# Optimization experiments

Hardware: AMD Instinct MI355X
Metric: run time of the kernel (lower is better)

## Reference

```python
import jax, jax.numpy as jnp
import numpy as np

B, H, W = 2, 64, 1024
C1, C2 = 64, 128
MLP = [128, 128]
KH, KW = 5, 5
NS = 3
DIST = 100.0
BN_EPS = 1e-5


def setup_inputs() -> dict:
    key = jax.random.key(0)
    ks = jax.random.split(key, 12)
    inp = {
        "xyz1_proj": jax.random.normal(ks[0], (B, H, W, 3), jnp.float32),
        "xyz2_proj": jax.random.normal(ks[1], (B, H, W, 3), jnp.float32),
        "feat1_proj": jax.random.normal(ks[2], (B, H, W, C1), jnp.float32),
        "feat2_proj": jax.random.normal(ks[3], (B, H, W, C2), jnp.float32),
    }
    cin = C1 + C2
    chans = [cin] + MLP
    for i in range(len(MLP)):
        inp[f"w{i}"] = jax.random.normal(ks[4 + 2 * i], (chans[i], chans[i + 1]), jnp.float32) * 0.05
        inp[f"b{i}"] = jnp.zeros((chans[i + 1],), jnp.float32)
        inp[f"g{i}"] = jnp.ones((chans[i + 1],), jnp.float32)
        inp[f"be{i}"] = jnp.zeros((chans[i + 1],), jnp.float32)
    return inp


def _grid_knn(xyz1, xyz2):
    """Structured-grid KNN (no_sort_knn): for each query pixel, scan a KHxKW
    window in row-major order and take the first NS in-bounds neighbors whose
    squared distance is below DIST^2. Returns flat neighbor indices (B,N,NS)
    and a validity mask (B,N,NS,1)."""
    b, h, w, _ = xyz1.shape
    n = h * w
    k = KH * KW
    x1 = xyz1.reshape(b, n, 3)
    x2 = xyz2.reshape(b, n, 3)
    oh = jnp.repeat(jnp.arange(KH) - KH // 2, KW)   # (K,)
    ow = jnp.tile(jnp.arange(KW) - KW // 2, KH)     # (K,)
    nh = jnp.arange(h)[:, None, None] + oh[None, None, :]   # (H,1,K)
    nw = jnp.arange(w)[None, :, None] + ow[None, None, :]   # (1,W,K)
    inb = ((nh >= 0) & (nh < h)) & ((nw >= 0) & (nw < w))    # (H,W,K)
    flat = jnp.clip(nh, 0, h - 1) * w + jnp.clip(nw, 0, w - 1)
    flat = jnp.broadcast_to(flat, (h, w, k)).reshape(n, k)
    inb = jnp.broadcast_to(inb, (h, w, k)).reshape(n, k)
    # window gather: (B,N,K,3)
    neigh = jnp.take(x2, flat.reshape(-1), axis=1).reshape(b, n, k, 3)
    sq = jnp.sum(jnp.square(neigh - x1[:, :, None, :]), -1)  # (B,N,K)
    valid = inb[None] & (sq < DIST * DIST)
    v = valid.astype(jnp.int32)
    rank = jnp.cumsum(v, -1) - v  # rank among valid, scan order
    sel, fnd = [], []
    for j in range(NS):
        hit = valid & (rank == j)
        sel.append(jnp.argmax(hit, -1))
        fnd.append(jnp.any(hit, -1))
    sel = jnp.stack(sel, -1)          # (B,N,NS) window slot
    found = jnp.stack(fnd, -1)        # (B,N,NS)
    flat_b = jnp.broadcast_to(flat[None], (b, n, k))
    sel_flat = jnp.take_along_axis(flat_b, sel, axis=-1)
    sel_flat = jnp.where(found, sel_flat, 0)  # zeros like the init buffers
    mask = found.astype(x1.dtype)[..., None]  # (B,N,NS,1)
    return sel_flat, mask


def _gather(feat_flat, sel_flat):
    # feat_flat: (B,N,C), sel_flat: (B,N,NS) -> (B,N,NS,C)
    b, n, c = feat_flat.shape
    idx = sel_flat.reshape(b, n * NS, 1)
    g = jnp.take_along_axis(feat_flat, jnp.broadcast_to(idx, (b, n * NS, c)), axis=1)
    return g.reshape(b, n, NS, c)


def reference(xyz1_proj, xyz2_proj, feat1_proj, feat2_proj,
              w0, b0, g0, be0, w1, b1, g1, be1):
    b, h, w, _ = xyz1_proj.shape
    n = h * w
    xyz1 = xyz1_proj.reshape(b, n, 3)
    xyz2 = xyz2_proj.reshape(b, n, 3)
    feat2 = feat2_proj.reshape(b, n, -1)

    sel_flat, mask = _grid_knn(xyz1_proj, xyz2_proj)
    mask = jax.lax.stop_gradient(mask)

    grouped_xyz = _gather(xyz2, sel_flat) * mask          # (B,N,NS,3)
    grouped_feat = _gather(feat2, sel_flat) * mask        # (B,N,NS,C2)

    dist = jnp.sum(jnp.square(grouped_xyz - xyz1[:, :, None, :]), -1)  # (B,N,NS)
    dist = jnp.where(dist < 1e-10, jnp.full_like(dist, 1e-10), dist)
    norm = jnp.sum(1.0 / dist, axis=2, keepdims=True)     # (B,N,1)
    weight = (1.0 / dist) / norm                          # (B,N,NS)
    interp = jnp.sum(grouped_feat * weight[..., None], axis=2)  # (B,N,C2)

    x = jnp.concatenate([feat1_proj.reshape(b, n, -1), interp], -1)  # (B,N,C1+C2)

    # 1x1 conv MLP with training-mode BatchNorm + ReLU
    for (wi, bi, gi, bei) in ((w0, b0, g0, be0), (w1, b1, g1, be1)):
        x = x @ wi + bi
        mu = jnp.mean(x, axis=(0, 1))
        var = jnp.var(x, axis=(0, 1))
        x = (x - mu) * jax.lax.rsqrt(var + BN_EPS) * gi + bei
        x = jax.nn.relu(x)
    return x  # (B, H*W, MLP[-1])
```

## Files before the change

### kernel.cpp

```cpp
#include <hip/hip_runtime.h>

#define H_    64
#define W_    1024
#define NPT   65536
#define NTOT  131072
#define C1_   64
#define C2_   128
#define CIN_  192
#define CM_   128
#define NS_   3
#define DIST2_ 10000.0f
#define BN_EPS_ 1e-5f
#define NSLOT 32

typedef __attribute__((ext_vector_type(8))) short short8;
typedef __attribute__((ext_vector_type(4))) float floatx4;

static __device__ __forceinline__ unsigned short f2bf(float f) {
    unsigned int u = __float_as_uint(f);
    u += 0x7fffu + ((u >> 16) & 1u);
    return (unsigned short)(u >> 16);
}
static __device__ __forceinline__ float bflo(unsigned u) { return __uint_as_float(u << 16); }
static __device__ __forceinline__ float bfhi(unsigned u) { return __uint_as_float(u & 0xffff0000u); }
static __device__ __forceinline__ unsigned packbf(float a, float b) {
    return (unsigned)f2bf(a) | ((unsigned)f2bf(b) << 16);
}

__global__ __launch_bounds__(256) void prep_knn_kernel(
    const float* __restrict__ w0, const float* __restrict__ w1,
    const float* __restrict__ xyz1, const float* __restrict__ xyz2,
    unsigned short* __restrict__ w0F, unsigned short* __restrict__ w1F,
    int* __restrict__ sel, float* __restrict__ wgt)
{
    const int blk = blockIdx.x;
    if (blk < 20) {
        int tid = blk * 256 + threadIdx.x;
        if (tid < 3072) {
            int c = tid, lane = c & 63, nt = (c >> 6) & 7, kk = c >> 9;
            int n = nt * 16 + (lane & 15);
            int kb = kk * 32 + (lane >> 4) * 8;
            #pragma unroll
            for (int j = 0; j < 8; j++)
                w0F[(size_t)c * 8 + j] = f2bf(w0[(size_t)(kb + j) * CM_ + n]);
        } else if (tid < 5120) {
            int c = tid - 3072, lane = c & 63, nt = (c >> 6) & 7, kk = c >> 9;
            int n = nt * 16 + (lane & 15);
            int kb = kk * 32 + (lane >> 4) * 8;
            #pragma unroll
            for (int j = 0; j < 8; j++)
                w1F[(size_t)c * 8 + j] = f2bf(w1[(size_t)(kb + j) * CM_ + n]);
        }
        return;
    }

    int pt = (blk - 20) * 256 + threadIdx.x;
    if (pt >= NTOT) return;
    int bidx = pt / NPT, n = pt % NPT;
    int h = n / W_, w = n % W_;

    const float* p1 = xyz1 + (size_t)pt * 3;
    float x1 = p1[0], y1 = p1[1], z1 = p1[2];
    const float* x2b = xyz2 + (size_t)bidx * NPT * 3;

    int   s0 = 0, s1 = 0, s2 = 0;
    float d0 = 0.f, d1 = 0.f, d2 = 0.f;
    int cnt = 0;
    for (int dh = -2; dh <= 2; dh++) {
        int nh = h + dh;
        bool okh = (nh >= 0) && (nh < H_);
        for (int dw = -2; dw <= 2; dw++) {
            int nw = w + dw;
            if (!(okh && nw >= 0 && nw < W_)) continue;
            int nidx = nh * W_ + nw;
            const float* p2 = x2b + (size_t)nidx * 3;
            float dx = p2[0] - x1, dy = p2[1] - y1, dz = p2[2] - z1;
            float sq = dx * dx + dy * dy + dz * dz;
            if (sq < DIST2_ && cnt < NS_) {
                if (cnt == 0)      { s0 = nidx; d0 = sq; }
                else if (cnt == 1) { s1 = nidx; d1 = sq; }
                else               { s2 = nidx; d2 = sq; }
                cnt++;
            }
        }
    }
    float self2 = x1 * x1 + y1 * y1 + z1 * z1;
    float dd0 = (cnt > 0) ? d0 : self2;
    float dd1 = (cnt > 1) ? d1 : self2;
    float dd2 = (cnt > 2) ? d2 : self2;
    dd0 = fmaxf(dd0, 1e-10f); dd1 = fmaxf(dd1, 1e-10f); dd2 = fmaxf(dd2, 1e-10f);
    float i0 = 1.0f / dd0, i1 = 1.0f / dd1, i2 = 1.0f / dd2;
    float norm = i0 + i1 + i2;
    sel[(size_t)pt * NS_ + 0] = (cnt > 0) ? s0 : 0;
    sel[(size_t)pt * NS_ + 1] = (cnt > 1) ? s1 : 0;
    sel[(size_t)pt * NS_ + 2] = (cnt > 2) ? s2 : 0;
    wgt[(size_t)pt * NS_ + 0] = (cnt > 0) ? i0 / norm : 0.f;
    wgt[(size_t)pt * NS_ + 1] = (cnt > 1) ? i1 / norm : 0.f;
    wgt[(size_t)pt * NS_ + 2] = (cnt > 2) ? i2 / norm : 0.f;
}

__global__ __launch_bounds__(256) void fused1_kernel(
    const float* __restrict__ feat1, const float* __restrict__ feat2,
    const int* __restrict__ sel, const float* __restrict__ wgt,
    const unsigned short* __restrict__ w0F, const float* __restrict__ b0,
    uint2* __restrict__ y0w, float* __restrict__ slots0)
{
    __shared__ unsigned short xstage[64][CIN_ + 8];
    __shared__ int   selL[64][NS_];
    __shared__ float wgtL[64][NS_];
    __shared__ float wsum[4][CM_], wsq[4][CM_];

    const int t = threadIdx.x;
    const int blk = blockIdx.x;
    const int pbase = blk * 64;
    const int bidx = blk >> 10;

    if (t < 64 * NS_) {
        ((int*)selL)[t]   = sel[(size_t)pbase * NS_ + t];
        ((float*)wgtL)[t] = wgt[(size_t)pbase * NS_ + t];
    }
    __syncthreads();

    #pragma unroll
    for (int i = 0; i < 4; i++) {
        int idx = t + i * 256;
        int p = idx >> 4, c4 = (idx & 15) << 2;
        float4 f = *(const float4*)(feat1 + (size_t)(pbase + p) * C1_ + c4);
        ushort4 u;
        u.x = f2bf(f.x); u.y = f2bf(f.y); u.z = f2bf(f.z); u.w = f2bf(f.w);
        *(ushort4*)&xstage[p][c4] = u;
    }
    const float* f2b = feat2 + (size_t)bidx * NPT * C2_;
    #pragma unroll
    for (int i = 0; i < 8; i++) {
        int idx = t + i * 256;
        int p = idx >> 5, c4 = (idx & 31) << 2;
        float ax = 0.f, ay = 0.f, az = 0.f, aw = 0.f;
        #pragma unroll
        for (int j = 0; j < NS_; j++) {
            float wj = wgtL[p][j];
            const float4 f = *(const float4*)(f2b + (size_t)selL[p][j] * C2_ + c4);
            ax += wj * f.x; ay += wj * f.y; az += wj * f.z; aw += wj * f.w;
        }
        ushort4 u;
        u.x = f2bf(ax); u.y = f2bf(ay); u.z = f2bf(az); u.w = f2bf(aw);
        *(ushort4*)&xstage[p][C1_ + c4] = u;
    }
    __syncthreads();

    const int wv = t >> 6, lane = t & 63;
    const int m = lane & 15, q = lane >> 4;
    const unsigned short* arow = &xstage[wv * 16 + m][q * 8];

    floatx4 acc[8];
    #pragma unroll
    for (int nt = 0; nt < 8; nt++) acc[nt] = (floatx4){0.f, 0.f, 0.f, 0.f};

    #pragma unroll
    for (int kk = 0; kk < 6; kk++) {
        short8 a = *(const short8*)(arow + kk * 32);
        #pragma unroll
        for (int nt = 0; nt < 8; nt++) {
            short8 bw = *(const short8*)(w0F + ((size_t)(kk * 8 + nt) * 64 + lane) * 8);
            acc[nt] = __builtin_amdgcn_mfma_f32_16x16x32_bf16(a, bw, acc[nt], 0, 0, 0);
        }
    }

    #pragma unroll
    for (int nt = 0; nt < 8; nt++) {
        int n = nt * 16 + m;
        float bv = b0[n];
        unsigned u0 = packbf(acc[nt][0] + bv, acc[nt][1] + bv);
        unsigned u1 = packbf(acc[nt][2] + bv, acc[nt][3] + bv);
        y0w[((size_t)(blk * 4 + wv) * 8 + nt) * 64 + lane] = make_uint2(u0, u1);
        float v0 = bflo(u0), v1 = bfhi(u0), v2 = bflo(u1), v3 = bfhi(u1);
        float s  = v0 + v1 + v2 + v3;
        float q2 = v0 * v0 + v1 * v1 + v2 * v2 + v3 * v3;
        s += __shfl_xor(s, 16, 64); q2 += __shfl_xor(q2, 16, 64);
        s += __shfl_xor(s, 32, 64); q2 += __shfl_xor(q2, 32, 64);
        if (q == 0) { wsum[wv][n] = s; wsq[wv][n] = q2; }
    }
    __syncthreads();

    float* slot = slots0 + (size_t)(blk & (NSLOT - 1)) * 256;
    if (t < CM_)
        atomicAdd(&slot[t], wsum[0][t] + wsum[1][t] + wsum[2][t] + wsum[3][t]);
    else
        atomicAdd(&slot[t], wsq[0][t - CM_] + wsq[1][t - CM_] + wsq[2][t - CM_] + wsq[3][t - CM_]);
}

__global__ __launch_bounds__(256) void fused2_kernel(
    const uint2* __restrict__ y0w, const float* __restrict__ slots0,
    const float* __restrict__ g0, const float* __restrict__ be0,
    const unsigned short* __restrict__ w1F, const float* __restrict__ b1,
    uint2* __restrict__ y1w, float* __restrict__ slots1)
{
    __shared__ unsigned short x1s[64][CM_ + 8];
    __shared__ float scl[CM_], shf[CM_];
    __shared__ float wsum[4][CM_], wsq[4][CM_];

    const int t = threadIdx.x;
    const int blk = blockIdx.x;

    if (t < CM_) {
        float s = 0.f, q2 = 0.f;
        #pragma unroll
        for (int sl = 0; sl < NSLOT; sl++) {
            s  += slots0[sl * 256 + t];
            q2 += slots0[sl * 256 + CM_ + t];
        }
        const float invn = 1.0f / (float)NTOT;
        float mu = s * invn, var = q2 * invn - mu * mu;
        float sc = g0[t] * rsqrtf(var + BN_EPS_);
        scl[t] = sc; shf[t] = be0[t] - mu * sc;
    }
    __syncthreads();

    const int wv = t >> 6, lane = t & 63;
    const int m = lane & 15, q = lane >> 4;
    float sclv[8], shfv[8];
    #pragma unroll
    for (int nt = 0; nt < 8; nt++) {
        sclv[nt] = scl[nt * 16 + m];
        shfv[nt] = shf[nt * 16 + m];
    }

    #pragma unroll
    for (int nt = 0; nt < 8; nt++) {
        uint2 u = y0w[((size_t)(blk * 4 + wv) * 8 + nt) * 64 + lane];
        float v0 = fmaxf(bflo(u.x) * sclv[nt] + shfv[nt], 0.f);
        float v1 = fmaxf(bfhi(u.x) * sclv[nt] + shfv[nt], 0.f);
        float v2 = fmaxf(bflo(u.y) * sclv[nt] + shfv[nt], 0.f);
        float v3 = fmaxf(bfhi(u.y) * sclv[nt] + shfv[nt], 0.f);
        int col = nt * 16 + m, rb = wv * 16 + q * 4;
        x1s[rb + 0][col] = f2bf(v0);
        x1s[rb + 1][col] = f2bf(v1);
        x1s[rb + 2][col] = f2bf(v2);
        x1s[rb + 3][col] = f2bf(v3);
    }
    __syncthreads();

    const unsigned short* arow = &x1s[wv * 16 + m][q * 8];
    floatx4 acc[8];
    #pragma unroll
    for (int nt = 0; nt < 8; nt++) acc[nt] = (floatx4){0.f, 0.f, 0.f, 0.f};

    #pragma unroll
    for (int kk = 0; kk < 4; kk++) {
        short8 a = *(const short8*)(arow + kk * 32);
        #pragma unroll
        for (int nt = 0; nt < 8; nt++) {
            short8 bw = *(const short8*)(w1F + ((size_t)(kk * 8 + nt) * 64 + lane) * 8);
            acc[nt] = __builtin_amdgcn_mfma_f32_16x16x32_bf16(a, bw, acc[nt], 0, 0, 0);
        }
    }

    #pragma unroll
    for (int nt = 0; nt < 8; nt++) {
        int n = nt * 16 + m;
        float bv = b1[n];
        unsigned u0 = packbf(acc[nt][0] + bv, acc[nt][1] + bv);
        unsigned u1 = packbf(acc[nt][2] + bv, acc[nt][3] + bv);
        y1w[((size_t)(blk * 4 + wv) * 8 + nt) * 64 + lane] = make_uint2(u0, u1);
        float v0 = bflo(u0), v1 = bfhi(u0), v2 = bflo(u1), v3 = bfhi(u1);
        float s  = v0 + v1 + v2 + v3;
        float q2 = v0 * v0 + v1 * v1 + v2 * v2 + v3 * v3;
        s += __shfl_xor(s, 16, 64); q2 += __shfl_xor(q2, 16, 64);
        s += __shfl_xor(s, 32, 64); q2 += __shfl_xor(q2, 32, 64);
        if (q == 0) { wsum[wv][n] = s; wsq[wv][n] = q2; }
    }
    __syncthreads();

    float* slot = slots1 + (size_t)(blk & (NSLOT - 1)) * 256;
    if (t < CM_)
        atomicAdd(&slot[t], wsum[0][t] + wsum[1][t] + wsum[2][t] + wsum[3][t]);
    else
        atomicAdd(&slot[t], wsq[0][t - CM_] + wsq[1][t - CM_] + wsq[2][t - CM_] + wsq[3][t - CM_]);
}

__global__ __launch_bounds__(256) void bn_out_kernel(
    const uint2* __restrict__ y1w, const float* __restrict__ slots1,
    const float* __restrict__ g1, const float* __restrict__ be1,
    float* __restrict__ out)
{
    __shared__ float scl[CM_], shf[CM_];
    const int t = threadIdx.x;
    const int blk = blockIdx.x;

    if (t < CM_) {
        float s = 0.f, q2 = 0.f;
        #pragma unroll
        for (int sl = 0; sl < NSLOT; sl++) {
            s  += slots1[sl * 256 + t];
            q2 += slots1[sl * 256 + CM_ + t];
        }
        const float invn = 1.0f / (float)NTOT;
        float mu = s * invn, var = q2 * invn - mu * mu;
        float sc = g1[t] * rsqrtf(var + BN_EPS_);
        scl[t] = sc; shf[t] = be1[t] - mu * sc;
    }
    __syncthreads();

    const int wv = t >> 6, lane = t & 63;
    const int m = lane & 15, q = lane >> 4;

    #pragma unroll
    for (int nt = 0; nt < 8; nt++) {
        uint2 u = y1w[((size_t)(blk * 4 + wv) * 8 + nt) * 64 + lane];
        int n = nt * 16 + m;
        float sc = scl[n], sh = shf[n];
        int rb = blk * 64 + wv * 16 + q * 4;
        out[(size_t)(rb + 0) * CM_ + n] = fmaxf(bflo(u.x) * sc + sh, 0.f);
        out[(size_t)(rb + 1) * CM_ + n] = fmaxf(bfhi(u.x) * sc + sh, 0.f);
        out[(size_t)(rb + 2) * CM_ + n] = fmaxf(bflo(u.y) * sc + sh, 0.f);
        out[(size_t)(rb + 3) * CM_ + n] = fmaxf(bfhi(u.y) * sc + sh, 0.f);
    }
}

extern "C" void kernel_launch(void* const* d_in, const int* in_sizes, int n_in,
                              void* d_out, int out_size, void* d_ws, size_t ws_size,
                              hipStream_t stream)
{
    const float* xyz1  = (const float*)d_in[0];
    const float* xyz2  = (const float*)d_in[1];
    const float* feat1 = (const float*)d_in[2];
    const float* feat2 = (const float*)d_in[3];
    const float* w0    = (const float*)d_in[4];
    const float* b0    = (const float*)d_in[5];
    const float* g0    = (const float*)d_in[6];
    const float* be0   = (const float*)d_in[7];
    const float* w1    = (const float*)d_in[8];
    const float* b1    = (const float*)d_in[9];
    const float* g1    = (const float*)d_in[10];
    const float* be1   = (const float*)d_in[11];
    float* out = (float*)d_out;

    char* ws = (char*)d_ws;
    float* slots0       = (float*)(ws);
    float* slots1       = (float*)(ws + (size_t)NSLOT * 256 * 4);
    char*  p            = ws + 2 * (size_t)NSLOT * 256 * 4;
    int*   sel          = (int*)p;             p += (size_t)NTOT * NS_ * 4;
    float* wgt          = (float*)p;           p += (size_t)NTOT * NS_ * 4;
    unsigned short* w0F = (unsigned short*)p;  p += (size_t)CIN_ * CM_ * 2;
    unsigned short* w1F = (unsigned short*)p;  p += (size_t)CM_ * CM_ * 2;
    uint2* y0w          = (uint2*)p;           p += (size_t)NTOT * CM_ * 2;
    uint2* y1w          = (uint2*)p;

    hipMemsetAsync(ws, 0, 2 * (size_t)NSLOT * 256 * 4, stream);

    prep_knn_kernel<<<20 + NTOT / 256, 256, 0, stream>>>(w0, w1, xyz1, xyz2,
                                                         w0F, w1F, sel, wgt);
    fused1_kernel<<<NTOT / 64, 256, 0, stream>>>(feat1, feat2, sel, wgt,
                                                 w0F, b0, y0w, slots0);
    fused2_kernel<<<NTOT / 64, 256, 0, stream>>>(y0w, slots0, g0, be0,
                                                 w1F, b1, y1w, slots1);
    bn_out_kernel<<<NTOT / 64, 256, 0, stream>>>(y1w, slots1, g1, be1, out);
}
```

Baseline: 227.6 us.

## Load MFMA A-fragments directly from global and hoist BN finalize into tiny kernel

Result: slower. 240.8 us (+5.8%).

```diff
diff --git a/kernel.cpp b/kernel.cpp
--- a/kernel.cpp
+++ b/kernel.cpp
@@ -99,58 +99,79 @@
     wgt[(size_t)pt * NS_ + 2] = (cnt > 2) ? i2 / norm : 0.f;
 }
 
-__global__ __launch_bounds__(256) void fused1_kernel(
+__global__ __launch_bounds__(128) void bnfin_kernel(
+    const float* __restrict__ slots, const float* __restrict__ g,
+    const float* __restrict__ be, float* __restrict__ bnp)
+{
+    int t = threadIdx.x;
+    float s = 0.f, q2 = 0.f;
+    #pragma unroll
+    for (int sl = 0; sl < NSLOT; sl++) {
+        s  += slots[sl * 256 + t];
+        q2 += slots[sl * 256 + CM_ + t];
+    }
+    const float invn = 1.0f / (float)NTOT;
+    float mu = s * invn, var = q2 * invn - mu * mu;
+    float sc = g[t] * rsqrtf(var + BN_EPS_);
+    bnp[t] = sc;
+    bnp[CM_ + t] = be[t] - mu * sc;
+}
+
+__global__ __launch_bounds__(256, 4) void fused1_kernel(
     const float* __restrict__ feat1, const float* __restrict__ feat2,
     const int* __restrict__ sel, const float* __restrict__ wgt,
     const unsigned short* __restrict__ w0F, const float* __restrict__ b0,
     uint2* __restrict__ y0w, float* __restrict__ slots0)
 {
-    __shared__ unsigned short xstage[64][CIN_ + 8];
-    __shared__ int   selL[64][NS_];
-    __shared__ float wgtL[64][NS_];
     __shared__ float wsum[4][CM_], wsq[4][CM_];
 
     const int t = threadIdx.x;
     const int blk = blockIdx.x;
     const int pbase = blk * 64;
     const int bidx = blk >> 10;
-
-    if (t < 64 * NS_) {
-        ((int*)selL)[t]   = sel[(size_t)pbase * NS_ + t];
-        ((float*)wgtL)[t] = wgt[(size_t)pbase * NS_ + t];
-    }
-    __syncthreads();
-
-    #pragma unroll
-    for (int i = 0; i < 4; i++) {
-        int idx = t + i * 256;
-        int p = idx >> 4, c4 = (idx & 15) << 2;
-        float4 f = *(const float4*)(feat1 + (size_t)(pbase + p) * C1_ + c4);
-        ushort4 u;
-        u.x = f2bf(f.x); u.y = f2bf(f.y); u.z = f2bf(f.z); u.w = f2bf(f.w);
-        *(ushort4*)&xstage[p][c4] = u;
-    }
-    const float* f2b = feat2 + (size_t)bidx * NPT * C2_;
-    #pragma unroll
-    for (int i = 0; i < 8; i++) {
-        int idx = t + i * 256;
-        int p = idx >> 5, c4 = (idx & 31) << 2;
-        float ax = 0.f, ay = 0.f, az = 0.f, aw = 0.f;
-        #pragma unroll
-        for (int j = 0; j < NS_; j++) {
-            float wj = wgtL[p][j];
-            const float4 f = *(const float4*)(f2b + (size_t)selL[p][j] * C2_ + c4);
-            ax += wj * f.x; ay += wj * f.y; az += wj * f.z; aw += wj * f.w;
-        }
-        ushort4 u;
-        u.x = f2bf(ax); u.y = f2bf(ay); u.z = f2bf(az); u.w = f2bf(aw);
-        *(ushort4*)&xstage[p][C1_ + c4] = u;
-    }
-    __syncthreads();
-
     const int wv = t >> 6, lane = t & 63;
     const int m = lane & 15, q = lane >> 4;
-    const unsigned short* arow = &xstage[wv * 16 + m][q * 8];
+    const int row = pbase + wv * 16 + m;
+
+    int   s0 = sel[(size_t)row * NS_ + 0];
+    int   s1 = sel[(size_t)row * NS_ + 1];
+    int   s2 = sel[(size_t)row * NS_ + 2];
+    float g0v = wgt[(size_t)row * NS_ + 0];
+    float g1v = wgt[(size_t)row * NS_ + 1];
+    float g2v = wgt[(size_t)row * NS_ + 2];
+    const float* f2b = feat2 + (size_t)bidx * NPT * C2_;
+    const float* r0 = f2b + (size_t)s0 * C2_;
+    const float* r1 = f2b + (size_t)s1 * C2_;
+    const float* r2 = f2b + (size_t)s2 * C2_;
+
+    short8 afrag[6];
+    #pragma unroll
+    for (int kk = 0; kk < 2; kk++) {
+        const float* src = feat1 + (size_t)row * C1_ + kk * 32 + q * 8;
+        float4 fa = *(const float4*)(src);
+        float4 fb = *(const float4*)(src + 4);
+        short8 a;
+        a[0] = f2bf(fa.x); a[1] = f2bf(fa.y); a[2] = f2bf(fa.z); a[3] = f2bf(fa.w);
+        a[4] = f2bf(fb.x); a[5] = f2bf(fb.y); a[6] = f2bf(fb.z); a[7] = f2bf(fb.w);
+        afrag[kk] = a;
+    }
+    #pragma unroll
+    for (int kc = 0; kc < 4; kc++) {
+        int ci = kc * 32 + q * 8;
+        float4 a0 = *(const float4*)(r0 + ci), a1 = *(const float4*)(r0 + ci + 4);
+        float4 c0 = *(const float4*)(r1 + ci), c1 = *(const float4*)(r1 + ci + 4);
+        float4 e0 = *(const float4*)(r2 + ci), e1 = *(const float4*)(r2 + ci + 4);
+        short8 a;
+        a[0] = f2bf(g0v * a0.x + g1v * c0.x + g2v * e0.x);
+        a[1] = f2bf(g0v * a0.y + g1v * c0.y + g2v * e0.y);
+        a[2] = f2bf(g0v * a0.z + g1v * c0.z + g2v * e0.z);
+        a[3] = f2bf(g0v * a0.w + g1v * c0.w + g2v * e0.w);
+        a[4] = f2bf(g0v * a1.x + g1v * c1.x + g2v * e1.x);
+        a[5] = f2bf(g0v * a1.y + g1v * c1.y + g2v * e1.y);
+        a[6] = f2bf(g0v * a1.z + g1v * c1.z + g2v * e1.z);
+        a[7] = f2bf(g0v * a1.w + g1v * c1.w + g2v * e1.w);
+        afrag[2 + kc] = a;
+    }
 
     floatx4 acc[8];
     #pragma unroll
@@ -158,11 +179,10 @@
 
     #pragma unroll
     for (int kk = 0; kk < 6; kk++) {
-        short8 a = *(const short8*)(arow + kk * 32);
         #pragma unroll
         for (int nt = 0; nt < 8; nt++) {
             short8 bw = *(const short8*)(w0F + ((size_t)(kk * 8 + nt) * 64 + lane) * 8);
-            acc[nt] = __builtin_amdgcn_mfma_f32_16x16x32_bf16(a, bw, acc[nt], 0, 0, 0);
+            acc[nt] = __builtin_amdgcn_mfma_f32_16x16x32_bf16(afrag[kk], bw, acc[nt], 0, 0, 0);
         }
     }
 
@@ -190,53 +210,32 @@
 }
 
 __global__ __launch_bounds__(256) void fused2_kernel(
-    const uint2* __restrict__ y0w, const float* __restrict__ slots0,
-    const float* __restrict__ g0, const float* __restrict__ be0,
+    const uint2* __restrict__ y0w, const float* __restrict__ bnp0,
     const unsigned short* __restrict__ w1F, const float* __restrict__ b1,
     uint2* __restrict__ y1w, float* __restrict__ slots1)
 {
     __shared__ unsigned short x1s[64][CM_ + 8];
-    __shared__ float scl[CM_], shf[CM_];
     __shared__ float wsum[4][CM_], wsq[4][CM_];
 
     const int t = threadIdx.x;
     const int blk = blockIdx.x;
-
-    if (t < CM_) {
-        float s = 0.f, q2 = 0.f;
-        #pragma unroll
-        for (int sl = 0; sl < NSLOT; sl++) {
-            s  += slots0[sl * 256 + t];
-            q2 += slots0[sl * 256 + CM_ + t];
-        }
-        const float invn = 1.0f / (float)NTOT;
-        float mu = s * invn, var = q2 * invn - mu * mu;
-        float sc = g0[t] * rsqrtf(var + BN_EPS_);
-        scl[t] = sc; shf[t] = be0[t] - mu * sc;
-    }
-    __syncthreads();
-
     const int wv = t >> 6, lane = t & 63;
     const int m = lane & 15, q = lane >> 4;
-    float sclv[8], shfv[8];
+
     #pragma unroll
     for (int nt = 0; nt < 8; nt++) {
-        sclv[nt] = scl[nt * 16 + m];
-        shfv[nt] = shf[nt * 16 + m];
-    }
-
-    #pragma unroll
-    for (int nt = 0; nt < 8; nt++) {
+        int n = nt * 16 + m;
+        float sc = bnp0[n], sh = bnp0[CM_ + n];
         uint2 u = y0w[((size_t)(blk * 4 + wv) * 8 + nt) * 64 + lane];
-        float v0 = fmaxf(bflo(u.x) * sclv[nt] + shfv[nt], 0.f);
-        float v1 = fmaxf(bfhi(u.x) * sclv[nt] + shfv[nt], 0.f);
-        float v2 = fmaxf(bflo(u.y) * sclv[nt] + shfv[nt], 0.f);
-        float v3 = fmaxf(bfhi(u.y) * sclv[nt] + shfv[nt], 0.f);
-        int col = nt * 16 + m, rb = wv * 16 + q * 4;
-        x1s[rb + 0][col] = f2bf(v0);
-        x1s[rb + 1][col] = f2bf(v1);
-        x1s[rb + 2][col] = f2bf(v2);
-        x1s[rb + 3][col] = f2bf(v3);
+        float v0 = fmaxf(bflo(u.x) * sc + sh, 0.f);
+        float v1 = fmaxf(bfhi(u.x) * sc + sh, 0.f);
+        float v2 = fmaxf(bflo(u.y) * sc + sh, 0.f);
+        float v3 = fmaxf(bfhi(u.y) * sc + sh, 0.f);
+        int rb = wv * 16 + q * 4;
+        x1s[rb + 0][n] = f2bf(v0);
+        x1s[rb + 1][n] = f2bf(v1);
+        x1s[rb + 2][n] = f2bf(v2);
+        x1s[rb + 3][n] = f2bf(v3);
     }
     __syncthreads();
 
@@ -279,36 +278,19 @@
 }
 
 __global__ __launch_bounds__(256) void bn_out_kernel(
-    const uint2* __restrict__ y1w, const float* __restrict__ slots1,
-    const float* __restrict__ g1, const float* __restrict__ be1,
+    const uint2* __restrict__ y1w, const float* __restrict__ bnp1,
     float* __restrict__ out)
 {
-    __shared__ float scl[CM_], shf[CM_];
     const int t = threadIdx.x;
     const int blk = blockIdx.x;
-
-    if (t < CM_) {
-        float s = 0.f, q2 = 0.f;
-        #pragma unroll
-        for (int sl = 0; sl < NSLOT; sl++) {
-            s  += slots1[sl * 256 + t];
-            q2 += slots1[sl * 256 + CM_ + t];
-        }
-        const float invn = 1.0f / (float)NTOT;
-        float mu = s * invn, var = q2 * invn - mu * mu;
-        float sc = g1[t] * rsqrtf(var + BN_EPS_);
-        scl[t] = sc; shf[t] = be1[t] - mu * sc;
-    }
-    __syncthreads();
-
     const int wv = t >> 6, lane = t & 63;
     const int m = lane & 15, q = lane >> 4;
 
     #pragma unroll
     for (int nt = 0; nt < 8; nt++) {
+        int n = nt * 16 + m;
+        float sc = bnp1[n], sh = bnp1[CM_ + n];
         uint2 u = y1w[((size_t)(blk * 4 + wv) * 8 + nt) * 64 + lane];
-        int n = nt * 16 + m;
-        float sc = scl[n], sh = shf[n];
         int rb = blk * 64 + wv * 16 + q * 4;
         out[(size_t)(rb + 0) * CM_ + n] = fmaxf(bflo(u.x) * sc + sh, 0.f);
         out[(size_t)(rb + 1) * CM_ + n] = fmaxf(bfhi(u.x) * sc + sh, 0.f);
@@ -338,7 +320,9 @@
     char* ws = (char*)d_ws;
     float* slots0       = (float*)(ws);
     float* slots1       = (float*)(ws + (size_t)NSLOT * 256 * 4);
-    char*  p            = ws + 2 * (size_t)NSLOT * 256 * 4;
+    float* bnp0         = (float*)(ws + 2 * (size_t)NSLOT * 256 * 4);
+    float* bnp1         = bnp0 + 256;
+    char*  p            = (char*)(bnp1 + 256);
     int*   sel          = (int*)p;             p += (size_t)NTOT * NS_ * 4;
     float* wgt          = (float*)p;           p += (size_t)NTOT * NS_ * 4;
     unsigned short* w0F = (unsigned short*)p;  p += (size_t)CIN_ * CM_ * 2;
@@ -352,7 +336,8 @@
                                                          w0F, w1F, sel, wgt);
     fused1_kernel<<<NTOT / 64, 256, 0, stream>>>(feat1, feat2, sel, wgt,
                                                  w0F, b0, y0w, slots0);
-    fused2_kernel<<<NTOT / 64, 256, 0, stream>>>(y0w, slots0, g0, be0,
-                                                 w1F, b1, y1w, slots1);
-    bn_out_kernel<<<NTOT / 64, 256, 0, stream>>>(y1w, slots1, g1, be1, out);
-}
+    bnfin_kernel<<<1, 128, 0, stream>>>(slots0, g0, be0, bnp0);
+    fused2_kernel<<<NTOT / 64, 256, 0, stream>>>(y0w, bnp0, w1F, b1, y1w, slots1);
+    bnfin_kernel<<<1, 128, 0, stream>>>(slots1, g1, be1, bnp1);
+    bn_out_kernel<<<NTOT / 64, 256, 0, stream>>>(y1w, bnp1, out);
+}
```
